# Optimization experiments

Measured on AMD Instinct MI355X. Metric: run time of the kernel, lower is better.

## Reference

```python
import jax, jax.numpy as jnp
import numpy as np

K = 3  # neighborhood kernel size (hard-coded by the view(B,H,W,3,3) in the source)
BIG_NEG = jnp.float32(-1e9)   # stand-in for -inf on masked neighbors (safe under softmax)
ROW_NEG = jnp.float32(-1e8)   # value used by the source for fully-occluded rows


def extract_local_patches(x, k=K):
    """x: [B,C,H,W] -> [B,C,H,W,k*k] with replicate padding (F.pad mode='replicate')."""
    p = k // 2
    xp = jnp.pad(x, ((0, 0), (0, 0), (p, p), (p, p)), mode='edge')
    B, C, H, W = x.shape
    shifts = [xp[:, :, i:i + H, j:j + W] for i in range(k) for j in range(k)]
    return jnp.stack(shifts, axis=-1)  # [B,C,H,W,k*k]


def setup_inputs() -> dict:
    key = jax.random.key(0)
    k1, k2, k3, k4 = jax.random.split(key, 4)
    B, C, H, W = 4, 640, 64, 64
    Ft = jax.random.normal(k1, (B, C, H, W), dtype=jnp.float32)
    Fwarp = jax.random.normal(k2, (B, C, H, W), dtype=jnp.float32)
    mask = jax.random.bernoulli(k3, 0.3, (B, 1, H, W)).astype(jnp.float32)
    conv_w = jax.random.normal(k4, (1, 2 * C), dtype=jnp.float32) * (1.0 / np.sqrt(2 * C))
    conv_b = jnp.zeros((1,), dtype=jnp.float32)
    return {"Ft": Ft, "Fwarp": Fwarp, "mask": mask, "conv_w": conv_w, "conv_b": conv_b}


def reference(Ft, Fwarp, mask, conv_w, conv_b):
    B, C, H, W = Ft.shape
    # 3x3 neighborhood of Fwarp: [B,C,H,W,9]
    Fp = extract_local_patches(Fwarp)
    # per-pixel dot product of Ft query with each of its 9 neighbors
    sim = jnp.einsum('bchw,bchwn->bhwn', Ft, Fp) / jnp.sqrt(jnp.float32(C))  # [B,H,W,9]
    # mask neighborhoods: [B,H,W,9]
    mp = extract_local_patches(mask)[:, 0]
    occluded = (mp == 1.0)
    sim = jnp.where(occluded, BIG_NEG, sim)
    # rows where every neighbor is occluded get a uniform large-negative row,
    # softmax'd then zeroed (matches masked_fill(-inf) -> -1e8 -> zero-out)
    valid = jnp.any(~occluded, axis=-1, keepdims=True)  # [B,H,W,1]
    sim = jnp.where(valid, sim, ROW_NEG)
    attn = jax.nn.softmax(sim, axis=-1)
    attn = jnp.where(valid, attn, 0.0)  # [B,H,W,9]
    # weighted sum over the 9 neighbors
    Fw = jnp.einsum('bchwn,bhwn->bchw', Fp, attn)  # [B,C,H,W]
    # lambda predictor: 1x1 conv + sigmoid over cat([Fwarp_weighted, Ft])
    x = jnp.concatenate([Fw, Ft], axis=1)  # [B,2C,H,W]
    lam = jax.nn.sigmoid(jnp.einsum('bihw,oi->bohw', x, conv_w) + conv_b[None, :, None, None])
    return lam * Ft + (1.0 - lam) * Fw
```

## Files before the change

kernel.cpp:

```cpp
#include <hip/hip_runtime.h>
#include <hip/hip_bf16.h>

#define B_  4
#define C_  640
#define H_  64
#define W_  64
#define G_  16
#define CPG 40
#define NT  1024

__device__ __forceinline__ unsigned short f2bf(float f) {
    __hip_bfloat16 h = __float2bfloat16(f);
    return __builtin_bit_cast(unsigned short, h);
}
__device__ __forceinline__ float bf2f(unsigned short u) {
    return __bfloat162float(__builtin_bit_cast(__hip_bfloat16, u));
}

__device__ __forceinline__ void row_acc(const float4 ft4, const float4 r,
                                        const int l16, float* a) {
    const float pw = __shfl_up(r.w, 1, 64);
    const float nx = __shfl_down(r.x, 1, 64);
    const float vL0 = (l16 == 0)  ? r.x : pw;
    const float vR3 = (l16 == 15) ? r.w : nx;
    a[0]  = fmaf(ft4.x, vL0, a[0]);
    a[1]  = fmaf(ft4.y, r.x, a[1]);
    a[2]  = fmaf(ft4.z, r.y, a[2]);
    a[3]  = fmaf(ft4.w, r.z, a[3]);
    a[4]  = fmaf(ft4.x, r.x, a[4]);
    a[5]  = fmaf(ft4.y, r.y, a[5]);
    a[6]  = fmaf(ft4.z, r.z, a[6]);
    a[7]  = fmaf(ft4.w, r.w, a[7]);
    a[8]  = fmaf(ft4.x, r.y, a[8]);
    a[9]  = fmaf(ft4.y, r.z, a[9]);
    a[10] = fmaf(ft4.z, r.w, a[10]);
    a[11] = fmaf(ft4.w, vR3, a[11]);
}

__device__ __forceinline__ void row_fw(const float4 r, const int l16,
                                       const float* at, const int r3,
                                       float* fwv) {
    const float pw = __shfl_up(r.w, 1, 64);
    const float nx = __shfl_down(r.x, 1, 64);
    const float vL0 = (l16 == 0)  ? r.x : pw;
    const float vR3 = (l16 == 15) ? r.w : nx;
    fwv[0] += at[0*9+r3]*vL0 + at[0*9+r3+1]*r.x + at[0*9+r3+2]*r.y;
    fwv[1] += at[1*9+r3]*r.x + at[1*9+r3+1]*r.y + at[1*9+r3+2]*r.z;
    fwv[2] += at[2*9+r3]*r.y + at[2*9+r3+1]*r.z + at[2*9+r3+2]*r.w;
    fwv[3] += at[3*9+r3]*r.z + at[3*9+r3+1]*r.w + at[3*9+r3+2]*vR3;
}

__global__ __launch_bounds__(NT, 4) void nca_fused(
    const float* __restrict__ Ft,
    const float* __restrict__ Fwp,
    const float* __restrict__ mask,
    const float* __restrict__ cw,
    const float* __restrict__ cb,
    float* __restrict__ out)
{
    __shared__ float lds_cw[2 * C_];
    __shared__ float lds_msk[3][W_];
    __shared__ float lds_sim[G_][W_][9];
    __shared__ float lds_attn[W_][9];
    __shared__ float lds_red[G_][W_];
    __shared__ float lds_lamT[W_];
    __shared__ float lds_lam[W_];
    __shared__ __hip_bfloat16 lds_fw[C_][W_];

    const int t   = threadIdx.x;
    const int l   = t & 63;
    const int g   = t >> 6;
    const int sub = l >> 4;
    const int l16 = l & 15;
    const int w0  = l16 * 4;

    const int n    = blockIdx.x + gridDim.x * blockIdx.y;
    const int slot = n >> 3;
    const int h = (n & 7) * 8 + (slot & 7);
    const int b = slot >> 3;

    const int hm = (h > 0) ? (h - 1) : 0;
    const int hp = (h < H_ - 1) ? (h + 1) : (H_ - 1);
    const size_t cs = (size_t)H_ * W_;
    const int c0 = g * CPG;

    for (int i = t; i < 2 * C_; i += NT) lds_cw[i] = cw[i];
    if (t < 3 * W_) {
        const int r = t >> 6, col = t & 63;
        const int row = (r == 0) ? hm : ((r == 1) ? h : hp);
        lds_msk[r][col] = mask[((size_t)b * H_ + row) * W_ + col];
    }
    __syncthreads();

    const size_t base = (size_t)(b * C_ + c0) * H_;
    const size_t lo   = (size_t)sub * cs + w0;
    const float* ftp = Ft  + (base + h ) * W_ + lo;
    const float* q0p = Fwp + (base + hm) * W_ + lo;
    const float* q1p = Fwp + (base + h ) * W_ + lo;
    const float* q2p = Fwp + (base + hp) * W_ + lo;

    float acc[36];
    #pragma unroll
    for (int i = 0; i < 36; ++i) acc[i] = 0.f;
    float lamT[4] = {0.f, 0.f, 0.f, 0.f};

    #pragma unroll 2
    for (int k = 0; k < CPG; k += 4) {
        const size_t off = (size_t)k * cs;
        const float4 ft4 = *(const float4*)(ftp + off);
        const float4 r0  = *(const float4*)(q0p + off);
        const float4 r1  = *(const float4*)(q1p + off);
        const float4 r2  = *(const float4*)(q2p + off);
        const float  wk  = lds_cw[C_ + c0 + k + sub];
        row_acc(ft4, r0, l16, &acc[0]);
        row_acc(ft4, r1, l16, &acc[12]);
        row_acc(ft4, r2, l16, &acc[24]);
        lamT[0] = fmaf(wk, ft4.x, lamT[0]);
        lamT[1] = fmaf(wk, ft4.y, lamT[1]);
        lamT[2] = fmaf(wk, ft4.z, lamT[2]);
        lamT[3] = fmaf(wk, ft4.w, lamT[3]);
    }

    #pragma unroll
    for (int i = 0; i < 36; ++i) {
        acc[i] += __shfl_xor(acc[i], 16, 64);
        acc[i] += __shfl_xor(acc[i], 32, 64);
    }
    #pragma unroll
    for (int px = 0; px < 4; ++px) {
        lamT[px] += __shfl_xor(lamT[px], 16, 64);
        lamT[px] += __shfl_xor(lamT[px], 32, 64);
    }

    if (l < 16) {
        #pragma unroll
        for (int px = 0; px < 4; ++px) {
            const int ww = w0 + px;
            #pragma unroll
            for (int rr = 0; rr < 3; ++rr) {
                lds_sim[g][ww][3*rr+0] = acc[(3*rr+0)*4 + px];
                lds_sim[g][ww][3*rr+1] = acc[(3*rr+1)*4 + px];
                lds_sim[g][ww][3*rr+2] = acc[(3*rr+2)*4 + px];
            }
            lds_red[g][ww] = lamT[px];
        }
    }
    __syncthreads();

    if (t < W_ * 9) {
        const int ww = t / 9, q = t % 9;
        float s = 0.f;
        #pragma unroll
        for (int gg = 0; gg < G_; ++gg) s += lds_sim[gg][ww][q];
        s *= 0.03952847075210474f;
        const int r = q / 3, j = q % 3;
        int col = ww + j - 1;
        col = col < 0 ? 0 : (col > W_ - 1 ? W_ - 1 : col);
        if (lds_msk[r][col] == 1.0f) s = -1e9f;
        lds_attn[ww][q] = s;
    }
    __syncthreads();

    if (t < W_) {
        float v[9];
        float mx = -3e38f;
        bool valid = false;
        #pragma unroll
        for (int q = 0; q < 9; ++q) {
            v[q] = lds_attn[t][q];
            if (v[q] > -5e8f) valid = true;
            mx = fmaxf(mx, v[q]);
        }
        float lt = 0.f;
        #pragma unroll
        for (int gg = 0; gg < G_; ++gg) lt += lds_red[gg][t];
        lds_lamT[t] = lt;
        if (!valid) {
            #pragma unroll
            for (int q = 0; q < 9; ++q) lds_attn[t][q] = 0.f;
        } else {
            float e[9], sum = 0.f;
            #pragma unroll
            for (int q = 0; q < 9; ++q) { e[q] = expf(v[q] - mx); sum += e[q]; }
            const float inv = 1.f / sum;
            #pragma unroll
            for (int q = 0; q < 9; ++q) lds_attn[t][q] = e[q] * inv;
        }
    }
    __syncthreads();

    float at[36];
    #pragma unroll
    for (int px = 0; px < 4; ++px)
        #pragma unroll
        for (int q = 0; q < 9; ++q) at[px*9+q] = lds_attn[w0+px][q];

    float lamF[4] = {0.f, 0.f, 0.f, 0.f};
    #pragma unroll 2
    for (int k = 0; k < CPG; k += 4) {
        const size_t off = (size_t)k * cs;
        const float4 r0 = *(const float4*)(q0p + off);
        const float4 r1 = *(const float4*)(q1p + off);
        const float4 r2 = *(const float4*)(q2p + off);
        float fwv[4] = {0.f, 0.f, 0.f, 0.f};
        row_fw(r0, l16, at, 0, fwv);
        row_fw(r1, l16, at, 3, fwv);
        row_fw(r2, l16, at, 6, fwv);
        const int c = c0 + k + sub;
        ushort4 us;
        us.x = f2bf(fwv[0]); us.y = f2bf(fwv[1]);
        us.z = f2bf(fwv[2]); us.w = f2bf(fwv[3]);
        *(ushort4*)(&lds_fw[c][w0]) = us;
        const float wk = lds_cw[c];
        lamF[0] = fmaf(wk, fwv[0], lamF[0]);
        lamF[1] = fmaf(wk, fwv[1], lamF[1]);
        lamF[2] = fmaf(wk, fwv[2], lamF[2]);
        lamF[3] = fmaf(wk, fwv[3], lamF[3]);
    }
    #pragma unroll
    for (int px = 0; px < 4; ++px) {
        lamF[px] += __shfl_xor(lamF[px], 16, 64);
        lamF[px] += __shfl_xor(lamF[px], 32, 64);
    }
    if (l < 16) {
        #pragma unroll
        for (int px = 0; px < 4; ++px) lds_red[g][w0+px] = lamF[px];
    }
    __syncthreads();

    if (t < W_) {
        float s = lds_lamT[t];
        #pragma unroll
        for (int gg = 0; gg < G_; ++gg) s += lds_red[gg][t];
        s += cb[0];
        lds_lam[t] = 1.f / (1.f + expf(-s));
    }
    __syncthreads();

    float lam4[4], oml4[4];
    #pragma unroll
    for (int px = 0; px < 4; ++px) {
        lam4[px] = lds_lam[w0 + px];
        oml4[px] = 1.f - lam4[px];
    }
    float* outp = out + (base + h) * W_ + lo;
    #pragma unroll 2
    for (int k = 0; k < CPG; k += 4) {
        const size_t off = (size_t)k * cs;
        const float4 ft4 = *(const float4*)(ftp + off);
        const ushort4 us = *(const ushort4*)(&lds_fw[c0 + k + sub][w0]);
        float4 o;
        o.x = lam4[0] * ft4.x + oml4[0] * bf2f(us.x);
        o.y = lam4[1] * ft4.y + oml4[1] * bf2f(us.y);
        o.z = lam4[2] * ft4.z + oml4[2] * bf2f(us.z);
        o.w = lam4[3] * ft4.w + oml4[3] * bf2f(us.w);
        *(float4*)(outp + off) = o;
    }
}

extern "C" void kernel_launch(void* const* d_in, const int* in_sizes, int n_in,
                              void* d_out, int out_size, void* d_ws, size_t ws_size,
                              hipStream_t stream) {
    const float* Ft   = (const float*)d_in[0];
    const float* Fwp  = (const float*)d_in[1];
    const float* mask = (const float*)d_in[2];
    const float* cw   = (const float*)d_in[3];
    const float* cb   = (const float*)d_in[4];
    float* out = (float*)d_out;

    dim3 grid(H_, B_);
    dim3 block(NT);
    nca_fused<<<grid, block, 0, stream>>>(Ft, Fwp, mask, cw, cb, out);
}
```

Baseline: 44.94 us.

## Split each row across two blocks with LDS halo columns

Each block now processes half an image row (32 pixels) with 512 threads. Each wave covers 80 channels using 8-lane groups of float4 columns, so the grid doubles to 512 blocks. The left and right neighbor columns at the half-row boundary are preloaded per channel into shared memory as a halo, and the mask tile is stored pre-clamped. This aims to spread work across more CUs and improve occupancy, at the cost of extra strided halo loads and an additional shuffle-reduction step.

```diff
diff --git a/kernel.cpp b/kernel.cpp
--- a/kernel.cpp
+++ b/kernel.cpp
@@ -1,13 +1,15 @@
 #include <hip/hip_runtime.h>
 #include <hip/hip_bf16.h>
 
-#define B_  4
-#define C_  640
-#define H_  64
-#define W_  64
-#define G_  16
-#define CPG 40
-#define NT  1024
+#define B_   4
+#define C_   640
+#define H_   64
+#define W_   64
+#define NT   512
+#define WVS  8
+#define PXB  32
+#define CPW  80
+#define FWP  36
 
 __device__ __forceinline__ unsigned short f2bf(float f) {
     __hip_bfloat16 h = __float2bfloat16(f);
@@ -18,11 +20,12 @@
 }
 
 __device__ __forceinline__ void row_acc(const float4 ft4, const float4 r,
-                                        const int l16, float* a) {
+                                        const int quad, const float hl, const float hr,
+                                        float* a) {
     const float pw = __shfl_up(r.w, 1, 64);
     const float nx = __shfl_down(r.x, 1, 64);
-    const float vL0 = (l16 == 0)  ? r.x : pw;
-    const float vR3 = (l16 == 15) ? r.w : nx;
+    const float vL0 = (quad == 0) ? hl : pw;
+    const float vR3 = (quad == 7) ? hr : nx;
     a[0]  = fmaf(ft4.x, vL0, a[0]);
     a[1]  = fmaf(ft4.y, r.x, a[1]);
     a[2]  = fmaf(ft4.z, r.y, a[2]);
@@ -37,13 +40,13 @@
     a[11] = fmaf(ft4.w, vR3, a[11]);
 }
 
-__device__ __forceinline__ void row_fw(const float4 r, const int l16,
-                                       const float* at, const int r3,
-                                       float* fwv) {
+__device__ __forceinline__ void row_fw(const float4 r, const int quad,
+                                       const float hl, const float hr,
+                                       const float* at, const int r3, float* fwv) {
     const float pw = __shfl_up(r.w, 1, 64);
     const float nx = __shfl_down(r.x, 1, 64);
-    const float vL0 = (l16 == 0)  ? r.x : pw;
-    const float vR3 = (l16 == 15) ? r.w : nx;
+    const float vL0 = (quad == 0) ? hl : pw;
+    const float vR3 = (quad == 7) ? hr : nx;
     fwv[0] += at[0*9+r3]*vL0 + at[0*9+r3+1]*r.x + at[0*9+r3+2]*r.y;
     fwv[1] += at[1*9+r3]*r.x + at[1*9+r3+1]*r.y + at[1*9+r3+2]*r.z;
     fwv[2] += at[2*9+r3]*r.y + at[2*9+r3+1]*r.z + at[2*9+r3+2]*r.w;
@@ -59,41 +62,59 @@
     float* __restrict__ out)
 {
     __shared__ float lds_cw[2 * C_];
-    __shared__ float lds_msk[3][W_];
-    __shared__ float lds_sim[G_][W_][9];
-    __shared__ float lds_attn[W_][9];
-    __shared__ float lds_red[G_][W_];
-    __shared__ float lds_lamT[W_];
-    __shared__ float lds_lam[W_];
-    __shared__ __hip_bfloat16 lds_fw[C_][W_];
-
-    const int t   = threadIdx.x;
-    const int l   = t & 63;
-    const int g   = t >> 6;
-    const int sub = l >> 4;
-    const int l16 = l & 15;
-    const int w0  = l16 * 4;
-
-    const int n    = blockIdx.x + gridDim.x * blockIdx.y;
-    const int slot = n >> 3;
-    const int h = (n & 7) * 8 + (slot & 7);
-    const int b = slot >> 3;
+    __shared__ float lds_msk[3][34];
+    __shared__ float lds_halo[3][2][C_];
+    __shared__ float lds_sim[WVS][PXB][9];
+    __shared__ float lds_attn[PXB][9];
+    __shared__ float lds_red[WVS][PXB];
+    __shared__ float lds_lamT[PXB];
+    __shared__ float lds_lam[PXB];
+    __shared__ __hip_bfloat16 lds_fw[C_][FWP];
+
+    const int t    = threadIdx.x;
+    const int l    = t & 63;
+    const int g    = t >> 6;
+    const int quad = l & 7;
+    const int sub  = l >> 3;
+    const int w0   = quad * 4;
+
+    const int n    = blockIdx.x;
+    const int xcd  = n & 7;
+    const int i    = n >> 3;
+    const int h    = xcd * 8 + (i & 7);
+    const int half = (i >> 3) & 1;
+    const int b    = i >> 4;
 
     const int hm = (h > 0) ? (h - 1) : 0;
     const int hp = (h < H_ - 1) ? (h + 1) : (H_ - 1);
+    const int colL = half * PXB;
     const size_t cs = (size_t)H_ * W_;
-    const int c0 = g * CPG;
-
-    for (int i = t; i < 2 * C_; i += NT) lds_cw[i] = cw[i];
-    if (t < 3 * W_) {
-        const int r = t >> 6, col = t & 63;
+    const int c0 = g * CPW;
+
+    for (int idx = t; idx < 2 * C_; idx += NT) lds_cw[idx] = cw[idx];
+    if (t < 3 * 34) {
+        const int r = t / 34, cl = t % 34;
+        int gcol = colL + cl - 1;
+        gcol = gcol < 0 ? 0 : (gcol > W_ - 1 ? W_ - 1 : gcol);
         const int row = (r == 0) ? hm : ((r == 1) ? h : hp);
-        lds_msk[r][col] = mask[((size_t)b * H_ + row) * W_ + col];
+        lds_msk[r][cl] = mask[((size_t)b * H_ + row) * W_ + gcol];
+    }
+    {
+        const int hcl = (colL > 0) ? colL - 1 : 0;
+        const int hcr = (colL + PXB < W_) ? colL + PXB : W_ - 1;
+        for (int idx = t; idx < 6 * C_; idx += NT) {
+            const int c = idx % C_;
+            const int rs = idx / C_;
+            const int r = rs >> 1, side = rs & 1;
+            const int row = (r == 0) ? hm : ((r == 1) ? h : hp);
+            const int gcol = side ? hcr : hcl;
+            lds_halo[r][side][c] = Fwp[((size_t)(b * C_ + c) * H_ + row) * W_ + gcol];
+        }
     }
     __syncthreads();
 
     const size_t base = (size_t)(b * C_ + c0) * H_;
-    const size_t lo   = (size_t)sub * cs + w0;
+    const size_t lo   = (size_t)sub * cs + colL + w0;
     const float* ftp = Ft  + (base + h ) * W_ + lo;
     const float* q0p = Fwp + (base + hm) * W_ + lo;
     const float* q1p = Fwp + (base + h ) * W_ + lo;
@@ -101,67 +122,64 @@
 
     float acc[36];
     #pragma unroll
-    for (int i = 0; i < 36; ++i) acc[i] = 0.f;
-    float lamT[4] = {0.f, 0.f, 0.f, 0.f};
+    for (int q = 0; q < 36; ++q) acc[q] = 0.f;
+    float lamT4[4] = {0.f, 0.f, 0.f, 0.f};
 
     #pragma unroll 2
-    for (int k = 0; k < CPG; k += 4) {
+    for (int k = 0; k < CPW; k += 8) {
         const size_t off = (size_t)k * cs;
         const float4 ft4 = *(const float4*)(ftp + off);
         const float4 r0  = *(const float4*)(q0p + off);
         const float4 r1  = *(const float4*)(q1p + off);
         const float4 r2  = *(const float4*)(q2p + off);
-        const float  wk  = lds_cw[C_ + c0 + k + sub];
-        row_acc(ft4, r0, l16, &acc[0]);
-        row_acc(ft4, r1, l16, &acc[12]);
-        row_acc(ft4, r2, l16, &acc[24]);
-        lamT[0] = fmaf(wk, ft4.x, lamT[0]);
-        lamT[1] = fmaf(wk, ft4.y, lamT[1]);
-        lamT[2] = fmaf(wk, ft4.z, lamT[2]);
-        lamT[3] = fmaf(wk, ft4.w, lamT[3]);
-    }
-
-    #pragma unroll
-    for (int i = 0; i < 36; ++i) {
-        acc[i] += __shfl_xor(acc[i], 16, 64);
-        acc[i] += __shfl_xor(acc[i], 32, 64);
+        const int c = c0 + k + sub;
+        const float wk = lds_cw[C_ + c];
+        row_acc(ft4, r0, quad, lds_halo[0][0][c], lds_halo[0][1][c], &acc[0]);
+        row_acc(ft4, r1, quad, lds_halo[1][0][c], lds_halo[1][1][c], &acc[12]);
+        row_acc(ft4, r2, quad, lds_halo[2][0][c], lds_halo[2][1][c], &acc[24]);
+        lamT4[0] = fmaf(wk, ft4.x, lamT4[0]);
+        lamT4[1] = fmaf(wk, ft4.y, lamT4[1]);
+        lamT4[2] = fmaf(wk, ft4.z, lamT4[2]);
+        lamT4[3] = fmaf(wk, ft4.w, lamT4[3]);
+    }
+
+    #pragma unroll
+    for (int q = 0; q < 36; ++q) {
+        acc[q] += __shfl_xor(acc[q], 8, 64);
+        acc[q] += __shfl_xor(acc[q], 16, 64);
+        acc[q] += __shfl_xor(acc[q], 32, 64);
     }
     #pragma unroll
     for (int px = 0; px < 4; ++px) {
-        lamT[px] += __shfl_xor(lamT[px], 16, 64);
-        lamT[px] += __shfl_xor(lamT[px], 32, 64);
-    }
-
-    if (l < 16) {
-        #pragma unroll
-        for (int px = 0; px < 4; ++px) {
-            const int ww = w0 + px;
-            #pragma unroll
-            for (int rr = 0; rr < 3; ++rr) {
-                lds_sim[g][ww][3*rr+0] = acc[(3*rr+0)*4 + px];
-                lds_sim[g][ww][3*rr+1] = acc[(3*rr+1)*4 + px];
-                lds_sim[g][ww][3*rr+2] = acc[(3*rr+2)*4 + px];
-            }
-            lds_red[g][ww] = lamT[px];
-        }
-    }
-    __syncthreads();
-
-    if (t < W_ * 9) {
+        lamT4[px] += __shfl_xor(lamT4[px], 8, 64);
+        lamT4[px] += __shfl_xor(lamT4[px], 16, 64);
+        lamT4[px] += __shfl_xor(lamT4[px], 32, 64);
+    }
+
+    if (sub < 4) {
+        const int px = sub;
+        #pragma unroll
+        for (int r = 0; r < 3; ++r)
+            #pragma unroll
+            for (int cc = 0; cc < 3; ++cc)
+                lds_sim[g][w0 + px][r * 3 + cc] = acc[(r * 3 + cc) * 4 + px];
+        lds_red[g][w0 + px] = lamT4[px];
+    }
+    __syncthreads();
+
+    if (t < PXB * 9) {
         const int ww = t / 9, q = t % 9;
         float s = 0.f;
         #pragma unroll
-        for (int gg = 0; gg < G_; ++gg) s += lds_sim[gg][ww][q];
+        for (int gg = 0; gg < WVS; ++gg) s += lds_sim[gg][ww][q];
         s *= 0.03952847075210474f;
         const int r = q / 3, j = q % 3;
-        int col = ww + j - 1;
-        col = col < 0 ? 0 : (col > W_ - 1 ? W_ - 1 : col);
-        if (lds_msk[r][col] == 1.0f) s = -1e9f;
+        if (lds_msk[r][ww + j] == 1.0f) s = -1e9f;
         lds_attn[ww][q] = s;
     }
     __syncthreads();
 
-    if (t < W_) {
+    if (t < PXB) {
         float v[9];
         float mx = -3e38f;
         bool valid = false;
@@ -173,7 +191,7 @@
         }
         float lt = 0.f;
         #pragma unroll
-        for (int gg = 0; gg < G_; ++gg) lt += lds_red[gg][t];
+        for (int gg = 0; gg < WVS; ++gg) lt += lds_red[gg][t];
         lds_lamT[t] = lt;
         if (!valid) {
             #pragma unroll
@@ -193,45 +211,43 @@
     #pragma unroll
     for (int px = 0; px < 4; ++px)
         #pragma unroll
-        for (int q = 0; q < 9; ++q) at[px*9+q] = lds_attn[w0+px][q];
-
-    float lamF[4] = {0.f, 0.f, 0.f, 0.f};
+        for (int q = 0; q < 9; ++q) at[px * 9 + q] = lds_attn[w0 + px][q];
+
+    float lamF4[4] = {0.f, 0.f, 0.f, 0.f};
     #pragma unroll 2
-    for (int k = 0; k < CPG; k += 4) {
+    for (int k = 0; k < CPW; k += 8) {
         const size_t off = (size_t)k * cs;
         const float4 r0 = *(const float4*)(q0p + off);
         const float4 r1 = *(const float4*)(q1p + off);
         const float4 r2 = *(const float4*)(q2p + off);
+        const int c = c0 + k + sub;
         float fwv[4] = {0.f, 0.f, 0.f, 0.f};
-        row_fw(r0, l16, at, 0, fwv);
-        row_fw(r1, l16, at, 3, fwv);
-        row_fw(r2, l16, at, 6, fwv);
-        const int c = c0 + k + sub;
+        row_fw(r0, quad, lds_halo[0][0][c], lds_halo[0][1][c], at, 0, fwv);
+        row_fw(r1, quad, lds_halo[1][0][c], lds_halo[1][1][c], at, 3, fwv);
+        row_fw(r2, quad, lds_halo[2][0][c], lds_halo[2][1][c], at, 6, fwv);
         ushort4 us;
         us.x = f2bf(fwv[0]); us.y = f2bf(fwv[1]);
         us.z = f2bf(fwv[2]); us.w = f2bf(fwv[3]);
         *(ushort4*)(&lds_fw[c][w0]) = us;
         const float wk = lds_cw[c];
-        lamF[0] = fmaf(wk, fwv[0], lamF[0]);
-        lamF[1] = fmaf(wk, fwv[1], lamF[1]);
-        lamF[2] = fmaf(wk, fwv[2], lamF[2]);
-        lamF[3] = fmaf(wk, fwv[3], lamF[3]);
+        lamF4[0] = fmaf(wk, fwv[0], lamF4[0]);
+        lamF4[1] = fmaf(wk, fwv[1], lamF4[1]);
+        lamF4[2] = fmaf(wk, fwv[2], lamF4[2]);
+        lamF4[3] = fmaf(wk, fwv[3], lamF4[3]);
     }
     #pragma unroll
     for (int px = 0; px < 4; ++px) {
-        lamF[px] += __shfl_xor(lamF[px], 16, 64);
-        lamF[px] += __shfl_xor(lamF[px], 32, 64);
-    }
-    if (l < 16) {
-        #pragma unroll
-        for (int px = 0; px < 4; ++px) lds_red[g][w0+px] = lamF[px];
-    }
-    __syncthreads();
-
-    if (t < W_) {
+        lamF4[px] += __shfl_xor(lamF4[px], 8, 64);
+        lamF4[px] += __shfl_xor(lamF4[px], 16, 64);
+        lamF4[px] += __shfl_xor(lamF4[px], 32, 64);
+    }
+    if (sub < 4) lds_red[g][w0 + sub] = lamF4[sub];
+    __syncthreads();
+
+    if (t < PXB) {
         float s = lds_lamT[t];
         #pragma unroll
-        for (int gg = 0; gg < G_; ++gg) s += lds_red[gg][t];
+        for (int gg = 0; gg < WVS; ++gg) s += lds_red[gg][t];
         s += cb[0];
         lds_lam[t] = 1.f / (1.f + expf(-s));
     }
@@ -245,7 +261,7 @@
     }
     float* outp = out + (base + h) * W_ + lo;
     #pragma unroll 2
-    for (int k = 0; k < CPG; k += 4) {
+    for (int k = 0; k < CPW; k += 8) {
         const size_t off = (size_t)k * cs;
         const float4 ft4 = *(const float4*)(ftp + off);
         const ushort4 us = *(const ushort4*)(&lds_fw[c0 + k + sub][w0]);
@@ -268,7 +284,7 @@
     const float* cb   = (const float*)d_in[4];
     float* out = (float*)d_out;
 
-    dim3 grid(H_, B_);
+    dim3 grid(B_ * H_ * 2);
     dim3 block(NT);
     nca_fused<<<grid, block, 0, stream>>>(Ft, Fwp, mask, cw, cb, out);
 }
```

Result: slower. 67.29 us (+49.7%).

## Compute lambda via projected rows algebraically, recompute Fw in final pass

Applied to the files above, without the earlier changes.

The lambda logit term w·Fw is rewritten as a sum over the 9 attention weights times per-row projections of Fwarp onto conv weights (P), computed in a second pass before the softmax. This removes the bf16 Fw staging buffer in LDS (about 80KB) and the separate Fw pass with its extra reduction and barriers. The final output loop now recomputes Fw in full fp32 directly from re-read Fwarp rows. The cost is an extra pass over Ft and the Fwarp rows in the projection loop, plus more loads in the final loop. The much smaller LDS footprint may allow higher occupancy.

```diff
diff --git a/kernel.cpp b/kernel.cpp
--- a/kernel.cpp
+++ b/kernel.cpp
@@ -8,14 +8,6 @@
 #define G_  16
 #define CPG 40
 #define NT  1024
-
-__device__ __forceinline__ unsigned short f2bf(float f) {
-    __hip_bfloat16 h = __float2bfloat16(f);
-    return __builtin_bit_cast(unsigned short, h);
-}
-__device__ __forceinline__ float bf2f(unsigned short u) {
-    return __bfloat162float(__builtin_bit_cast(__hip_bfloat16, u));
-}
 
 __device__ __forceinline__ void row_acc(const float4 ft4, const float4 r,
                                         const int l16, float* a) {
@@ -38,8 +30,7 @@
 }
 
 __device__ __forceinline__ void row_fw(const float4 r, const int l16,
-                                       const float* at, const int r3,
-                                       float* fwv) {
+                                       const float* at, const int r3, float* fwv) {
     const float pw = __shfl_up(r.w, 1, 64);
     const float nx = __shfl_down(r.x, 1, 64);
     const float vL0 = (l16 == 0)  ? r.x : pw;
@@ -61,11 +52,10 @@
     __shared__ float lds_cw[2 * C_];
     __shared__ float lds_msk[3][W_];
     __shared__ float lds_sim[G_][W_][9];
+    __shared__ float lds_PT[G_][4][W_];
     __shared__ float lds_attn[W_][9];
-    __shared__ float lds_red[G_][W_];
-    __shared__ float lds_lamT[W_];
+    __shared__ float lds_Pf[4][W_];
     __shared__ float lds_lam[W_];
-    __shared__ __hip_bfloat16 lds_fw[C_][W_];
 
     const int t   = threadIdx.x;
     const int l   = t & 63;
@@ -102,7 +92,6 @@
     float acc[36];
     #pragma unroll
     for (int i = 0; i < 36; ++i) acc[i] = 0.f;
-    float lamT[4] = {0.f, 0.f, 0.f, 0.f};
 
     #pragma unroll 2
     for (int k = 0; k < CPG; k += 4) {
@@ -111,14 +100,35 @@
         const float4 r0  = *(const float4*)(q0p + off);
         const float4 r1  = *(const float4*)(q1p + off);
         const float4 r2  = *(const float4*)(q2p + off);
-        const float  wk  = lds_cw[C_ + c0 + k + sub];
         row_acc(ft4, r0, l16, &acc[0]);
         row_acc(ft4, r1, l16, &acc[12]);
         row_acc(ft4, r2, l16, &acc[24]);
-        lamT[0] = fmaf(wk, ft4.x, lamT[0]);
-        lamT[1] = fmaf(wk, ft4.y, lamT[1]);
-        lamT[2] = fmaf(wk, ft4.z, lamT[2]);
-        lamT[3] = fmaf(wk, ft4.w, lamT[3]);
+    }
+
+    float Pp[12], T4[4];
+    #pragma unroll
+    for (int i = 0; i < 12; ++i) Pp[i] = 0.f;
+    #pragma unroll
+    for (int i = 0; i < 4; ++i) T4[i] = 0.f;
+
+    #pragma unroll 2
+    for (int k = 0; k < CPG; k += 4) {
+        const size_t off = (size_t)k * cs;
+        const float4 ft4 = *(const float4*)(ftp + off);
+        const float4 r0  = *(const float4*)(q0p + off);
+        const float4 r1  = *(const float4*)(q1p + off);
+        const float4 r2  = *(const float4*)(q2p + off);
+        const int c = c0 + k + sub;
+        const float wF = lds_cw[c];
+        const float wT = lds_cw[C_ + c];
+        Pp[0] = fmaf(wF, r0.x, Pp[0]); Pp[1]  = fmaf(wF, r0.y, Pp[1]);
+        Pp[2] = fmaf(wF, r0.z, Pp[2]); Pp[3]  = fmaf(wF, r0.w, Pp[3]);
+        Pp[4] = fmaf(wF, r1.x, Pp[4]); Pp[5]  = fmaf(wF, r1.y, Pp[5]);
+        Pp[6] = fmaf(wF, r1.z, Pp[6]); Pp[7]  = fmaf(wF, r1.w, Pp[7]);
+        Pp[8] = fmaf(wF, r2.x, Pp[8]); Pp[9]  = fmaf(wF, r2.y, Pp[9]);
+        Pp[10]= fmaf(wF, r2.z, Pp[10]);Pp[11] = fmaf(wF, r2.w, Pp[11]);
+        T4[0] = fmaf(wT, ft4.x, T4[0]); T4[1] = fmaf(wT, ft4.y, T4[1]);
+        T4[2] = fmaf(wT, ft4.z, T4[2]); T4[3] = fmaf(wT, ft4.w, T4[3]);
     }
 
     #pragma unroll
@@ -127,23 +137,26 @@
         acc[i] += __shfl_xor(acc[i], 32, 64);
     }
     #pragma unroll
-    for (int px = 0; px < 4; ++px) {
-        lamT[px] += __shfl_xor(lamT[px], 16, 64);
-        lamT[px] += __shfl_xor(lamT[px], 32, 64);
-    }
-
-    if (l < 16) {
-        #pragma unroll
-        for (int px = 0; px < 4; ++px) {
-            const int ww = w0 + px;
-            #pragma unroll
-            for (int rr = 0; rr < 3; ++rr) {
-                lds_sim[g][ww][3*rr+0] = acc[(3*rr+0)*4 + px];
-                lds_sim[g][ww][3*rr+1] = acc[(3*rr+1)*4 + px];
-                lds_sim[g][ww][3*rr+2] = acc[(3*rr+2)*4 + px];
-            }
-            lds_red[g][ww] = lamT[px];
-        }
+    for (int i = 0; i < 12; ++i) {
+        Pp[i] += __shfl_xor(Pp[i], 16, 64);
+        Pp[i] += __shfl_xor(Pp[i], 32, 64);
+    }
+    #pragma unroll
+    for (int i = 0; i < 4; ++i) {
+        T4[i] += __shfl_xor(T4[i], 16, 64);
+        T4[i] += __shfl_xor(T4[i], 32, 64);
+    }
+
+    {
+        const int px = sub;
+        #pragma unroll
+        for (int r = 0; r < 3; ++r)
+            #pragma unroll
+            for (int cc = 0; cc < 3; ++cc)
+                lds_sim[g][w0 + px][r * 3 + cc] = acc[r * 12 + cc * 4 + px];
+        #pragma unroll
+        for (int r = 0; r < 3; ++r) lds_PT[g][r][w0 + px] = Pp[r * 4 + px];
+        lds_PT[g][3][w0 + px] = T4[px];
     }
     __syncthreads();
 
@@ -158,6 +171,13 @@
         col = col < 0 ? 0 : (col > W_ - 1 ? W_ - 1 : col);
         if (lds_msk[r][col] == 1.0f) s = -1e9f;
         lds_attn[ww][q] = s;
+    } else if (t >= 640 && t < 640 + 256) {
+        const int idx = t - 640;
+        const int r = idx >> 6, ww = idx & 63;
+        float s = 0.f;
+        #pragma unroll
+        for (int gg = 0; gg < G_; ++gg) s += lds_PT[gg][r][ww];
+        lds_Pf[r][ww] = s;
     }
     __syncthreads();
 
@@ -171,21 +191,32 @@
             if (v[q] > -5e8f) valid = true;
             mx = fmaxf(mx, v[q]);
         }
-        float lt = 0.f;
-        #pragma unroll
-        for (int gg = 0; gg < G_; ++gg) lt += lds_red[gg][t];
-        lds_lamT[t] = lt;
+        float a9[9];
         if (!valid) {
             #pragma unroll
-            for (int q = 0; q < 9; ++q) lds_attn[t][q] = 0.f;
+            for (int q = 0; q < 9; ++q) a9[q] = 0.f;
         } else {
-            float e[9], sum = 0.f;
-            #pragma unroll
-            for (int q = 0; q < 9; ++q) { e[q] = expf(v[q] - mx); sum += e[q]; }
+            float sum = 0.f;
+            #pragma unroll
+            for (int q = 0; q < 9; ++q) { a9[q] = expf(v[q] - mx); sum += a9[q]; }
             const float inv = 1.f / sum;
             #pragma unroll
-            for (int q = 0; q < 9; ++q) lds_attn[t][q] = e[q] * inv;
+            for (int q = 0; q < 9; ++q) a9[q] *= inv;
         }
+        #pragma unroll
+        for (int q = 0; q < 9; ++q) lds_attn[t][q] = a9[q];
+
+        float lamF = 0.f;
+        #pragma unroll
+        for (int r = 0; r < 3; ++r)
+            #pragma unroll
+            for (int j = 0; j < 3; ++j) {
+                int col = t + j - 1;
+                col = col < 0 ? 0 : (col > W_ - 1 ? W_ - 1 : col);
+                lamF = fmaf(a9[r * 3 + j], lds_Pf[r][col], lamF);
+            }
+        const float d = lds_Pf[3][t] + lamF + cb[0];
+        lds_lam[t] = 1.f / (1.f + expf(-d));
     }
     __syncthreads();
 
@@ -193,67 +224,31 @@
     #pragma unroll
     for (int px = 0; px < 4; ++px)
         #pragma unroll
-        for (int q = 0; q < 9; ++q) at[px*9+q] = lds_attn[w0+px][q];
-
-    float lamF[4] = {0.f, 0.f, 0.f, 0.f};
-    #pragma unroll 2
-    for (int k = 0; k < CPG; k += 4) {
-        const size_t off = (size_t)k * cs;
-        const float4 r0 = *(const float4*)(q0p + off);
-        const float4 r1 = *(const float4*)(q1p + off);
-        const float4 r2 = *(const float4*)(q2p + off);
-        float fwv[4] = {0.f, 0.f, 0.f, 0.f};
-        row_fw(r0, l16, at, 0, fwv);
-        row_fw(r1, l16, at, 3, fwv);
-        row_fw(r2, l16, at, 6, fwv);
-        const int c = c0 + k + sub;
-        ushort4 us;
-        us.x = f2bf(fwv[0]); us.y = f2bf(fwv[1]);
-        us.z = f2bf(fwv[2]); us.w = f2bf(fwv[3]);
-        *(ushort4*)(&lds_fw[c][w0]) = us;
-        const float wk = lds_cw[c];
-        lamF[0] = fmaf(wk, fwv[0], lamF[0]);
-        lamF[1] = fmaf(wk, fwv[1], lamF[1]);
-        lamF[2] = fmaf(wk, fwv[2], lamF[2]);
-        lamF[3] = fmaf(wk, fwv[3], lamF[3]);
-    }
-    #pragma unroll
-    for (int px = 0; px < 4; ++px) {
-        lamF[px] += __shfl_xor(lamF[px], 16, 64);
-        lamF[px] += __shfl_xor(lamF[px], 32, 64);
-    }
-    if (l < 16) {
-        #pragma unroll
-        for (int px = 0; px < 4; ++px) lds_red[g][w0+px] = lamF[px];
-    }
-    __syncthreads();
-
-    if (t < W_) {
-        float s = lds_lamT[t];
-        #pragma unroll
-        for (int gg = 0; gg < G_; ++gg) s += lds_red[gg][t];
-        s += cb[0];
-        lds_lam[t] = 1.f / (1.f + expf(-s));
-    }
-    __syncthreads();
-
+        for (int q = 0; q < 9; ++q) at[px * 9 + q] = lds_attn[w0 + px][q];
     float lam4[4], oml4[4];
     #pragma unroll
     for (int px = 0; px < 4; ++px) {
         lam4[px] = lds_lam[w0 + px];
         oml4[px] = 1.f - lam4[px];
     }
+
     float* outp = out + (base + h) * W_ + lo;
     #pragma unroll 2
     for (int k = 0; k < CPG; k += 4) {
         const size_t off = (size_t)k * cs;
         const float4 ft4 = *(const float4*)(ftp + off);
-        const ushort4 us = *(const ushort4*)(&lds_fw[c0 + k + sub][w0]);
+        const float4 r0  = *(const float4*)(q0p + off);
+        const float4 r1  = *(const float4*)(q1p + off);
+        const float4 r2  = *(const float4*)(q2p + off);
+        float fwv[4] = {0.f, 0.f, 0.f, 0.f};
+        row_fw(r0, l16, at, 0, fwv);
+        row_fw(r1, l16, at, 3, fwv);
+        row_fw(r2, l16, at, 6, fwv);
         float4 o;
-        o.x = lam4[0] * ft4.x + oml4[0] * bf2f(us.x);
-        o.y = lam4[1] * ft4.y + oml4[1] * bf2f(us.y);
-        o.z = lam4[2] * ft4.z + oml4[2] * bf2f(us.z);
-        o.w = lam4[3] * ft4.w + oml4[3] * bf2f(us.w);
+        o.x = lam4[0] * ft4.x + oml4[0] * fwv[0];
+        o.y = lam4[1] * ft4.y + oml4[1] * fwv[1];
+        o.z = lam4[2] * ft4.z + oml4[2] * fwv[2];
+        o.w = lam4[3] * ft4.w + oml4[3] * fwv[3];
         *(float4*)(outp + off) = o;
     }
 }
```

Measured after the change: 74.25 us. 65.2% more time.
